# Performance work log

Hardware: AMD Instinct MI355X
Metric: run time of the kernel (lower is better)

## Reference

```python
import jax, jax.numpy as jnp
import numpy as np

B, S, IN_DIM, D, H, L = 2, 2048, 64, 512, 8, 2
DK = D // H
EPS = 1e-5

def _layernorm(x, g, b):
    mu = jnp.mean(x, axis=-1, keepdims=True)
    var = jnp.mean((x - mu) ** 2, axis=-1, keepdims=True)
    return (x - mu) * jax.lax.rsqrt(var + EPS) * g + b

def _prob_sparse_layer(x, Wq, bq, Wk, bk, Wv, bv, fcW, fcb, ln_g, ln_b):
    # x: [B, S, D]
    Bs, Ss, _ = x.shape
    Q = (x @ Wq + bq).reshape(Bs, Ss, H, DK).transpose(0, 2, 1, 3)  # [B,H,S,DK]
    K = (x @ Wk + bk).reshape(Bs, Ss, H, DK).transpose(0, 2, 1, 3)
    V = (x @ Wv + bv).reshape(Bs, Ss, H, DK).transpose(0, 2, 1, 3)
    scores = jnp.einsum('bhqd,bhkd->bhqk', Q, K) / np.sqrt(DK).astype(np.float32)
    k = max(1, Ss // 10)
    top_scores, _ = jax.lax.top_k(scores, k)          # [B,H,S,k]
    threshold = top_scores[..., -1:]                  # k-th largest per row
    sparse_scores = jnp.where(scores < threshold, -jnp.inf, scores)
    attn = jax.nn.softmax(sparse_scores, axis=-1)     # dropout is identity in eval
    out = jnp.einsum('bhqk,bhkd->bhqd', attn, V)
    out = out.transpose(0, 2, 1, 3).reshape(Bs, Ss, D)
    out = out @ fcW + fcb
    return _layernorm(x + out, ln_g, ln_b)

def setup_inputs() -> dict:
    key = jax.random.key(0)
    ks = jax.random.split(key, 16)
    sd = 1.0 / np.sqrt(D)
    sdi = 1.0 / np.sqrt(IN_DIM)
    return {
        'x': jax.random.normal(ks[0], (B, S, IN_DIM), jnp.float32),
        'enc_W': jax.random.normal(ks[1], (IN_DIM, D), jnp.float32) * sdi,
        'enc_b': jnp.zeros((D,), jnp.float32),
        'Wq': jax.random.normal(ks[2], (L, D, D), jnp.float32) * sd,
        'bq': jnp.zeros((L, D), jnp.float32),
        'Wk': jax.random.normal(ks[3], (L, D, D), jnp.float32) * sd,
        'bk': jnp.zeros((L, D), jnp.float32),
        'Wv': jax.random.normal(ks[4], (L, D, D), jnp.float32) * sd,
        'bv': jnp.zeros((L, D), jnp.float32),
        'fcW': jax.random.normal(ks[5], (L, D, D), jnp.float32) * sd,
        'fcb': jnp.zeros((L, D), jnp.float32),
        'ln_g': jnp.ones((L, D), jnp.float32),
        'ln_b': jnp.zeros((L, D), jnp.float32),
        'dec_W': jax.random.normal(ks[6], (D, IN_DIM), jnp.float32) * sd,
        'dec_b': jnp.zeros((IN_DIM,), jnp.float32),
    }

def reference(x, enc_W, enc_b, Wq, bq, Wk, bk, Wv, bv, fcW, fcb, ln_g, ln_b, dec_W, dec_b):
    h = x @ enc_W + enc_b  # [B,S,D]
    for i in range(Wq.shape[0]):
        h = _prob_sparse_layer(h, Wq[i], bq[i], Wk[i], bk[i], Wv[i], bv[i],
                               fcW[i], fcb[i], ln_g[i], ln_b[i])
    return h[:, -1, :] @ dec_W + dec_b  # [B, IN_DIM]
```

## Files before the change

### kernel.cpp

```cpp
#include <hip/hip_runtime.h>
#include <hip/hip_bf16.h>

typedef unsigned short u16;
typedef __bf16 bf16x8 __attribute__((ext_vector_type(8)));
typedef u16 u16x8 __attribute__((ext_vector_type(8)));
typedef float f32x4 __attribute__((ext_vector_type(4)));

#define S_LEN 2048
#define NH 8
#define DMODEL 512
#define TOPK 204

__device__ __forceinline__ u16 f2b(float f) {
  __hip_bfloat16 h = __float2bfloat16(f);
  return __builtin_bit_cast(u16, h);
}
__device__ __forceinline__ unsigned kmap16(u16 b) {
  return (unsigned)(u16)(b ^ ((b & 0x8000) ? 0xFFFFu : 0x8000u));
}
__device__ __forceinline__ float kunmap(unsigned k) {
  unsigned tb = (k & 0x8000u) ? (k ^ 0x8000u) : (~k & 0xFFFFu);
  return __uint_as_float(tb << 16);
}

__global__ void transpose_w(const float* __restrict__ in, u16* __restrict__ out, int R, int C) {
  __shared__ float tile[32][33];
  int c0 = blockIdx.x * 32, r0 = blockIdx.y * 32;
  int tx = threadIdx.x & 31, ty = threadIdx.x >> 5;
#pragma unroll
  for (int i = 0; i < 32; i += 8)
    tile[ty + i][tx] = in[(long long)(r0 + ty + i) * C + c0 + tx];
  __syncthreads();
#pragma unroll
  for (int i = 0; i < 32; i += 8)
    out[(long long)(c0 + ty + i) * R + r0 + tx] = f2b(tile[tx][ty + i]);
}

__global__ void transpose_w4(const float* __restrict__ W0, const float* __restrict__ W1,
                             const float* __restrict__ W2, const float* __restrict__ W3,
                             u16* __restrict__ O0, u16* __restrict__ O1,
                             u16* __restrict__ O2, u16* __restrict__ O3) {
  __shared__ float tile[32][33];
  const float* in;
  u16* out;
  switch (blockIdx.z) {
    case 0: in = W0; out = O0; break;
    case 1: in = W1; out = O1; break;
    case 2: in = W2; out = O2; break;
    default: in = W3; out = O3; break;
  }
  int c0 = blockIdx.x * 32, r0 = blockIdx.y * 32;
  int tx = threadIdx.x & 31, ty = threadIdx.x >> 5;
#pragma unroll
  for (int i = 0; i < 32; i += 8)
    tile[ty + i][tx] = in[(long long)(r0 + ty + i) * 512 + c0 + tx];
  __syncthreads();
#pragma unroll
  for (int i = 0; i < 32; i += 8)
    out[(long long)(c0 + ty + i) * 512 + r0 + tx] = f2b(tile[tx][ty + i]);
}

__global__ void conv_b(const float* __restrict__ in, u16* __restrict__ out, int n) {
  int i = blockIdx.x * 256 + threadIdx.x;
  if (i < n) out[i] = f2b(i < n ? in[i] : 0.f);
}

template <int MODE>
__global__ __launch_bounds__(256) void gemm_bt(
    const u16* __restrict__ A, const u16* __restrict__ BT, const float* __restrict__ bias,
    float* __restrict__ outF, u16* __restrict__ outB,
    int M, int N, int K, float scale) {
  __shared__ u16 As[64 * 32];
  __shared__ u16 Bs[128 * 32];
  int n0 = blockIdx.x * 128, m0 = blockIdx.y * 64;
  int t = threadIdx.x;
  int lane = t & 63, wv = t >> 6;
  int mw = (wv & 1) * 32, nw = (wv >> 1) * 64;
  int fr = lane & 15, fg = lane >> 4;
  f32x4 acc[2][4] = {};
  for (int kt = 0; kt < K; kt += 32) {
    int e0 = t * 8;
    int r0r = e0 >> 5, c0c = e0 & 31;
    int e1 = e0 + 2048;
    int r1r = e1 >> 5, c1c = e1 & 31;
    *(u16x8*)&As[e0] = *(const u16x8*)&A[(long long)(m0 + r0r) * K + kt + c0c];
    *(u16x8*)&Bs[e0] = *(const u16x8*)&BT[(long long)(n0 + r0r) * K + kt + c0c];
    *(u16x8*)&Bs[e1] = *(const u16x8*)&BT[(long long)(n0 + r1r) * K + kt + c1c];
    __syncthreads();
    bf16x8 af[2], bfv[4];
#pragma unroll
    for (int i = 0; i < 2; i++) af[i] = *(const bf16x8*)&As[(mw + i * 16 + fr) * 32 + fg * 8];
#pragma unroll
    for (int j = 0; j < 4; j++) bfv[j] = *(const bf16x8*)&Bs[(nw + j * 16 + fr) * 32 + fg * 8];
#pragma unroll
    for (int i = 0; i < 2; i++)
#pragma unroll
      for (int j = 0; j < 4; j++)
        acc[i][j] = __builtin_amdgcn_mfma_f32_16x16x32_bf16(af[i], bfv[j], acc[i][j], 0, 0, 0);
    __syncthreads();
  }
#pragma unroll
  for (int i = 0; i < 2; i++)
#pragma unroll
    for (int j = 0; j < 4; j++) {
      int mloc = mw + i * 16 + fg * 4;
      int n = n0 + nw + j * 16 + fr;
      float bvl = bias ? bias[n] : 0.f;
#pragma unroll
      for (int r = 0; r < 4; r++) {
        int m = m0 + mloc + r;
        float v = acc[i][j][r] * scale + bvl;
        if constexpr (MODE == 0) {
          outF[(long long)m * N + n] = v;
        } else if constexpr (MODE == 4) {
          outF[(long long)m * N + n] = v;
          outB[(long long)m * N + n] = f2b(v);
        } else if constexpr (MODE == 2) {
          outB[(long long)((m >> 11) * NH + (n >> 6)) * (S_LEN * 64) + (long long)(m & 2047) * 64 + (n & 63)] = f2b(v);
        } else if constexpr (MODE == 3) {
          outB[((long long)((m >> 11) * NH + (n >> 6)) * 64 + (n & 63)) * S_LEN + (m & 2047)] = f2b(v);
        }
      }
    }
}

__global__ __launch_bounds__(512) void score_pv(
    const u16* __restrict__ Qb, const u16* __restrict__ Kb, const u16* __restrict__ VTb,
    u16* __restrict__ aoB) {
  __shared__ u16 Qs[16 * 64];
  __shared__ u16 Ss[16 * 2048];
  __shared__ unsigned lokeyS[16];
  __shared__ float mS[16];
  __shared__ float zS[8 * 16];
  int bh = blockIdx.y, m0 = blockIdx.x * 16, t = threadIdx.x;
  int lane = t & 63, wv = t >> 6, fr = lane & 15, fg = lane >> 4;
  const u16* Qg = Qb + ((long long)bh * S_LEN + m0) * 64;
  const u16* Kg = Kb + (long long)bh * S_LEN * 64;
  const u16* Vg = VTb + (long long)bh * 64 * S_LEN;
  if (t < 128) {
    int row = t >> 3, cc = t & 7;
    *(u16x8*)&Qs[row * 64 + ((cc ^ (row & 7)) * 8)] = *(const u16x8*)&Qg[row * 64 + cc * 8];
  }
  __syncthreads();
  bf16x8 aq[2];
#pragma unroll
  for (int ks = 0; ks < 2; ks++)
    aq[ks] = *(const bf16x8*)&Qs[fr * 64 + (((fg + 4 * ks) ^ (fr & 7)) * 8)];

#pragma unroll 4
  for (int tt = 0; tt < 16; tt++) {
    int col0 = wv * 256 + tt * 16;
    f32x4 acc = {};
#pragma unroll
    for (int ks = 0; ks < 2; ks++) {
      bf16x8 bk = *(const bf16x8*)&Kg[(long long)(col0 + fr) * 64 + ks * 32 + fg * 8];
      acc = __builtin_amdgcn_mfma_f32_16x16x32_bf16(aq[ks], bk, acc, 0, 0, 0);
    }
#pragma unroll
    for (int r = 0; r < 4; r++) {
      float s = acc[r] * 0.125f;
      u16 key = (u16)kmap16(f2b(s));
      int row = fg * 4 + r;
      Ss[row * 2048 + ((col0 + fr) ^ ((row & 15) << 3))] = key;
    }
  }
  __syncthreads();

  for (int rr = wv * 2; rr < wv * 2 + 2; rr++) {
    const unsigned* cu = (const unsigned*)&Ss[rr * 2048];
    unsigned k32[32];
#pragma unroll
    for (int j = 0; j < 16; j++) {
      unsigned w = cu[lane + 64 * j];
      k32[2 * j] = w & 0xFFFFu;
      k32[2 * j + 1] = w >> 16;
    }
    unsigned mx = 0;
#pragma unroll
    for (int j = 0; j < 32; j++) mx = max(mx, k32[j]);
#pragma unroll
    for (int o = 1; o < 64; o <<= 1) mx = max(mx, (unsigned)__shfl_xor((int)mx, o));
    unsigned lo = 0, hi = mx;
    while (lo < hi) {
      unsigned mid = (lo + hi + 1) >> 1;
      int c = 0;
#pragma unroll
      for (int j = 0; j < 32; j++)
        c += (int)__popcll(__ballot(k32[j] >= mid));
      if (c >= TOPK) lo = mid; else hi = mid - 1;
    }
    if (lane == 0) {
      lokeyS[rr] = lo;
      mS[rr] = kunmap(mx);
    }
  }
  __syncthreads();

  unsigned myLo = lokeyS[fr];
  float myM = mS[fr];
  float zpart = 0.f;
  f32x4 acc_o[4] = {};
#pragma unroll 2
  for (int step = 0; step < 8; step++) {
    int k0 = wv * 256 + step * 32;
    u16x8 kk = *(const u16x8*)&Ss[fr * 2048 + ((k0 + fg * 8) ^ ((fr & 15) << 3))];
    u16x8 wpa;
#pragma unroll
    for (int e = 0; e < 8; e++) {
      unsigned key = kk[e];
      float pv = 0.f;
      if (key >= myLo) pv = __expf(kunmap(key) - myM);
      zpart += pv;
      wpa[e] = f2b(pv);
    }
    bf16x8 pa = *(bf16x8*)&wpa;
#pragma unroll
    for (int j = 0; j < 4; j++) {
      bf16x8 bv = *(const bf16x8*)&Vg[(long long)(j * 16 + fr) * 2048 + k0 + fg * 8];
      acc_o[j] = __builtin_amdgcn_mfma_f32_16x16x32_bf16(pa, bv, acc_o[j], 0, 0, 0);
    }
  }
  zpart += __shfl_xor(zpart, 16);
  zpart += __shfl_xor(zpart, 32);
  __syncthreads();

  float* Of = (float*)Ss;
#pragma unroll
  for (int j = 0; j < 4; j++)
#pragma unroll
    for (int r = 0; r < 4; r++)
      Of[wv * 1024 + (fg * 4 + r) * 64 + j * 16 + fr] = acc_o[j][r];
  if (fg == 0) zS[wv * 16 + fr] = zpart;
  __syncthreads();
  long long ob = (long long)(bh >> 3) * S_LEN * DMODEL + (bh & 7) * 64;
#pragma unroll
  for (int o = t; o < 1024; o += 512) {
    int row = o >> 6, dk = o & 63;
    float s = 0.f;
#pragma unroll
    for (int w = 0; w < 8; w++) s += Of[w * 1024 + o];
    float z = 0.f;
#pragma unroll
    for (int w = 0; w < 8; w++) z += zS[w * 16 + row];
    aoB[ob + (long long)(m0 + row) * DMODEL + dk] = f2b(s / z);
  }
}

__global__ __launch_bounds__(256) void resid_ln(const float* __restrict__ h, const float* __restrict__ fco,
                                                const float* __restrict__ g, const float* __restrict__ b,
                                                float* __restrict__ hout, u16* __restrict__ hbout) {
  __shared__ float red[4];
  int row = blockIdx.x;
  int t = threadIdx.x;
  long long base = (long long)row * 512;
  float v0 = h[base + t] + fco[base + t];
  float v1 = h[base + t + 256] + fco[base + t + 256];
  float s = v0 + v1;
#pragma unroll
  for (int o = 32; o > 0; o >>= 1) s += __shfl_down(s, o);
  if ((t & 63) == 0) red[t >> 6] = s;
  __syncthreads();
  float mu = (red[0] + red[1] + red[2] + red[3]) * (1.f / 512.f);
  float d0 = v0 - mu, d1 = v1 - mu;
  float q = d0 * d0 + d1 * d1;
#pragma unroll
  for (int o = 32; o > 0; o >>= 1) q += __shfl_down(q, o);
  __syncthreads();
  if ((t & 63) == 0) red[t >> 6] = q;
  __syncthreads();
  float var = (red[0] + red[1] + red[2] + red[3]) * (1.f / 512.f);
  float rs = rsqrtf(var + 1e-5f);
  float y0 = d0 * rs * g[t] + b[t];
  float y1 = d1 * rs * g[t + 256] + b[t + 256];
  hout[base + t] = y0;
  hout[base + t + 256] = y1;
  hbout[base + t] = f2b(y0);
  hbout[base + t + 256] = f2b(y1);
}

__global__ void decoder_k(const float* __restrict__ h, const float* __restrict__ W,
                          const float* __restrict__ bias, float* __restrict__ out) {
  int t = threadIdx.x;
  int b = t >> 6, j = t & 63;
  const float* hr = h + ((long long)b * S_LEN + (S_LEN - 1)) * DMODEL;
  float s = 0.f;
  for (int d = 0; d < DMODEL; d++) s += hr[d] * W[(long long)d * 64 + j];
  out[t] = s + bias[j];
}

extern "C" void kernel_launch(void* const* d_in, const int* in_sizes, int n_in,
                              void* d_out, int out_size, void* d_ws, size_t ws_size,
                              hipStream_t stream) {
  const float* x = (const float*)d_in[0];
  const float* enc_W = (const float*)d_in[1];
  const float* enc_b = (const float*)d_in[2];
  const float* Wq = (const float*)d_in[3];
  const float* bq = (const float*)d_in[4];
  const float* Wk = (const float*)d_in[5];
  const float* bk = (const float*)d_in[6];
  const float* Wv = (const float*)d_in[7];
  const float* bv = (const float*)d_in[8];
  const float* fcW = (const float*)d_in[9];
  const float* fcb = (const float*)d_in[10];
  const float* ln_g = (const float*)d_in[11];
  const float* ln_b = (const float*)d_in[12];
  const float* dec_W = (const float*)d_in[13];
  const float* dec_b = (const float*)d_in[14];

  char* p = (char*)d_ws;
  auto alloc = [&](size_t bytes) {
    char* r = p;
    p += (bytes + 255) & ~(size_t)255;
    return r;
  };
  const size_t BS = 2 * (size_t)S_LEN;
  u16* encWT = (u16*)alloc(512 * 64 * 2);
  u16* xbf = (u16*)alloc(BS * 64 * 2);
  float* hF = (float*)alloc(BS * 512 * 4);
  u16* hB = (u16*)alloc(BS * 512 * 2);
  u16* WqT = (u16*)alloc(512 * 512 * 2);
  u16* WkT = (u16*)alloc(512 * 512 * 2);
  u16* WvT = (u16*)alloc(512 * 512 * 2);
  u16* fcWT = (u16*)alloc(512 * 512 * 2);
  u16* Qb = (u16*)alloc((size_t)16 * 2048 * 64 * 2);
  u16* Kb = (u16*)alloc((size_t)16 * 2048 * 64 * 2);
  u16* VTb = (u16*)alloc((size_t)16 * 2048 * 64 * 2);
  u16* aoB = (u16*)alloc(BS * 512 * 2);
  float* fcO = (float*)Qb;

  transpose_w<<<dim3(16, 2), 256, 0, stream>>>(enc_W, encWT, 64, 512);
  conv_b<<<(int)(BS * 64 / 256), 256, 0, stream>>>(x, xbf, (int)(BS * 64));
  gemm_bt<4><<<dim3(4, 64), 256, 0, stream>>>(xbf, encWT, enc_b, hF, hB, 4096, 512, 64, 1.f);

  for (int l = 0; l < 2; l++) {
    transpose_w4<<<dim3(16, 16, 4), 256, 0, stream>>>(
        Wq + (size_t)l * 512 * 512, Wk + (size_t)l * 512 * 512,
        Wv + (size_t)l * 512 * 512, fcW + (size_t)l * 512 * 512,
        WqT, WkT, WvT, fcWT);
    gemm_bt<2><<<dim3(4, 64), 256, 0, stream>>>(hB, WqT, bq + l * 512, nullptr, Qb, 4096, 512, 512, 1.f);
    gemm_bt<2><<<dim3(4, 64), 256, 0, stream>>>(hB, WkT, bk + l * 512, nullptr, Kb, 4096, 512, 512, 1.f);
    gemm_bt<3><<<dim3(4, 64), 256, 0, stream>>>(hB, WvT, bv + l * 512, nullptr, VTb, 4096, 512, 512, 1.f);
    score_pv<<<dim3(128, 16), 512, 0, stream>>>(Qb, Kb, VTb, aoB);
    gemm_bt<0><<<dim3(4, 64), 256, 0, stream>>>(aoB, fcWT, fcb + l * 512, fcO, nullptr, 4096, 512, 512, 1.f);
    resid_ln<<<4096, 256, 0, stream>>>(hF, fcO, ln_g + l * 512, ln_b + l * 512, hF, hB);
  }
  decoder_k<<<1, 128, 0, stream>>>(hF, dec_W, dec_b, (float*)d_out);
}
```

Before: 447.5 us.

## Fuse QKV projections into one GEMM and double score_pv waves per block

Replaces three separate Q, K and V projection launches with one GEMM over N=1536. It picks the bias and the output layout per 512-column segment. This relies on WqT, WkT and WvT being laid out contiguously in memory. The attention kernel now runs 1024 threads per block, so each wave handles one row's top-k binary search and half as many score and PV columns. The partial-output reduction goes through a swizzled shared buffer to avoid bank conflicts. The aim is fewer launches, better reuse of the A tile, and more parallelism in the selection phase, at the cost of higher register pressure and a wider cross-wave reduction.

```diff
diff --git a/kernel.cpp b/kernel.cpp
--- a/kernel.cpp
+++ b/kernel.cpp
@@ -62,13 +62,14 @@
 
 __global__ void conv_b(const float* __restrict__ in, u16* __restrict__ out, int n) {
   int i = blockIdx.x * 256 + threadIdx.x;
-  if (i < n) out[i] = f2b(i < n ? in[i] : 0.f);
+  if (i < n) out[i] = f2b(in[i]);
 }
 
 template <int MODE>
 __global__ __launch_bounds__(256) void gemm_bt(
-    const u16* __restrict__ A, const u16* __restrict__ BT, const float* __restrict__ bias,
-    float* __restrict__ outF, u16* __restrict__ outB,
+    const u16* __restrict__ A, const u16* __restrict__ BT,
+    const float* __restrict__ bias, const float* __restrict__ biasK, const float* __restrict__ biasV,
+    float* __restrict__ outF, u16* __restrict__ outB, u16* __restrict__ outBK, u16* __restrict__ outBV,
     int M, int N, int K, float scale) {
   __shared__ u16 As[64 * 32];
   __shared__ u16 Bs[128 * 32];
@@ -105,7 +106,13 @@
     for (int j = 0; j < 4; j++) {
       int mloc = mw + i * 16 + fg * 4;
       int n = n0 + nw + j * 16 + fr;
-      float bvl = bias ? bias[n] : 0.f;
+      float bvl;
+      if constexpr (MODE == 5) {
+        int seg = n >> 9, nn = n & 511;
+        bvl = (seg == 0 ? bias : seg == 1 ? biasK : biasV)[nn];
+      } else {
+        bvl = bias ? bias[n] : 0.f;
+      }
 #pragma unroll
       for (int r = 0; r < 4; r++) {
         int m = m0 + mloc + r;
@@ -115,23 +122,30 @@
         } else if constexpr (MODE == 4) {
           outF[(long long)m * N + n] = v;
           outB[(long long)m * N + n] = f2b(v);
-        } else if constexpr (MODE == 2) {
-          outB[(long long)((m >> 11) * NH + (n >> 6)) * (S_LEN * 64) + (long long)(m & 2047) * 64 + (n & 63)] = f2b(v);
-        } else if constexpr (MODE == 3) {
-          outB[((long long)((m >> 11) * NH + (n >> 6)) * 64 + (n & 63)) * S_LEN + (m & 2047)] = f2b(v);
+        } else if constexpr (MODE == 5) {
+          int seg = n >> 9, nn = n & 511;
+          u16 val = f2b(v);
+          if (seg == 2) {
+            outBV[((long long)((m >> 11) * NH + (nn >> 6)) * 64 + (nn & 63)) * S_LEN + (m & 2047)] = val;
+          } else {
+            long long qkidx = (long long)((m >> 11) * NH + (nn >> 6)) * (S_LEN * 64) +
+                              (long long)(m & 2047) * 64 + (nn & 63);
+            if (seg == 0) outB[qkidx] = val;
+            else outBK[qkidx] = val;
+          }
         }
       }
     }
 }
 
-__global__ __launch_bounds__(512) void score_pv(
+__global__ __launch_bounds__(1024, 8) void score_pv(
     const u16* __restrict__ Qb, const u16* __restrict__ Kb, const u16* __restrict__ VTb,
     u16* __restrict__ aoB) {
   __shared__ u16 Qs[16 * 64];
-  __shared__ u16 Ss[16 * 2048];
+  __shared__ __align__(16) u16 Ss[16 * 2048];
   __shared__ unsigned lokeyS[16];
   __shared__ float mS[16];
-  __shared__ float zS[8 * 16];
+  __shared__ float zS[16 * 16];
   int bh = blockIdx.y, m0 = blockIdx.x * 16, t = threadIdx.x;
   int lane = t & 63, wv = t >> 6, fr = lane & 15, fg = lane >> 4;
   const u16* Qg = Qb + ((long long)bh * S_LEN + m0) * 64;
@@ -148,8 +162,8 @@
     aq[ks] = *(const bf16x8*)&Qs[fr * 64 + (((fg + 4 * ks) ^ (fr & 7)) * 8)];
 
 #pragma unroll 4
-  for (int tt = 0; tt < 16; tt++) {
-    int col0 = wv * 256 + tt * 16;
+  for (int tt = 0; tt < 8; tt++) {
+    int col0 = wv * 128 + tt * 16;
     f32x4 acc = {};
 #pragma unroll
     for (int ks = 0; ks < 2; ks++) {
@@ -166,7 +180,8 @@
   }
   __syncthreads();
 
-  for (int rr = wv * 2; rr < wv * 2 + 2; rr++) {
+  {
+    int rr = wv;
     const unsigned* cu = (const unsigned*)&Ss[rr * 2048];
     unsigned k32[32];
 #pragma unroll
@@ -201,8 +216,8 @@
   float zpart = 0.f;
   f32x4 acc_o[4] = {};
 #pragma unroll 2
-  for (int step = 0; step < 8; step++) {
-    int k0 = wv * 256 + step * 32;
+  for (int step = 0; step < 4; step++) {
+    int k0 = wv * 128 + step * 32;
     u16x8 kk = *(const u16x8*)&Ss[fr * 2048 + ((k0 + fg * 8) ^ ((fr & 15) << 3))];
     u16x8 wpa;
 #pragma unroll
@@ -228,20 +243,22 @@
 #pragma unroll
   for (int j = 0; j < 4; j++)
 #pragma unroll
-    for (int r = 0; r < 4; r++)
-      Of[wv * 1024 + (fg * 4 + r) * 64 + j * 16 + fr] = acc_o[j][r];
+    for (int r = 0; r < 4; r++) {
+      int row = fg * 4 + r, col = j * 16 + fr;
+      Of[wv * 1024 + row * 64 + (col ^ ((row >> 2) << 3))] = acc_o[j][r];
+    }
   if (fg == 0) zS[wv * 16 + fr] = zpart;
   __syncthreads();
   long long ob = (long long)(bh >> 3) * S_LEN * DMODEL + (bh & 7) * 64;
-#pragma unroll
-  for (int o = t; o < 1024; o += 512) {
-    int row = o >> 6, dk = o & 63;
+  {
+    int row = t >> 6, dk = t & 63;
+    int sw = dk ^ ((row >> 2) << 3);
     float s = 0.f;
 #pragma unroll
-    for (int w = 0; w < 8; w++) s += Of[w * 1024 + o];
+    for (int w = 0; w < 16; w++) s += Of[w * 1024 + row * 64 + sw];
     float z = 0.f;
 #pragma unroll
-    for (int w = 0; w < 8; w++) z += zS[w * 16 + row];
+    for (int w = 0; w < 16; w++) z += zS[w * 16 + row];
     aoB[ob + (long long)(m0 + row) * DMODEL + dk] = f2b(s / z);
   }
 }
@@ -330,18 +347,19 @@
 
   transpose_w<<<dim3(16, 2), 256, 0, stream>>>(enc_W, encWT, 64, 512);
   conv_b<<<(int)(BS * 64 / 256), 256, 0, stream>>>(x, xbf, (int)(BS * 64));
-  gemm_bt<4><<<dim3(4, 64), 256, 0, stream>>>(xbf, encWT, enc_b, hF, hB, 4096, 512, 64, 1.f);
+  gemm_bt<4><<<dim3(4, 64), 256, 0, stream>>>(xbf, encWT, enc_b, nullptr, nullptr,
+                                              hF, hB, nullptr, nullptr, 4096, 512, 64, 1.f);
 
   for (int l = 0; l < 2; l++) {
     transpose_w4<<<dim3(16, 16, 4), 256, 0, stream>>>(
         Wq + (size_t)l * 512 * 512, Wk + (size_t)l * 512 * 512,
         Wv + (size_t)l * 512 * 512, fcW + (size_t)l * 512 * 512,
         WqT, WkT, WvT, fcWT);
-    gemm_bt<2><<<dim3(4, 64), 256, 0, stream>>>(hB, WqT, bq + l * 512, nullptr, Qb, 4096, 512, 512, 1.f);
-    gemm_bt<2><<<dim3(4, 64), 256, 0, stream>>>(hB, WkT, bk + l * 512, nullptr, Kb, 4096, 512, 512, 1.f);
-    gemm_bt<3><<<dim3(4, 64), 256, 0, stream>>>(hB, WvT, bv + l * 512, nullptr, VTb, 4096, 512, 512, 1.f);
-    score_pv<<<dim3(128, 16), 512, 0, stream>>>(Qb, Kb, VTb, aoB);
-    gemm_bt<0><<<dim3(4, 64), 256, 0, stream>>>(aoB, fcWT, fcb + l * 512, fcO, nullptr, 4096, 512, 512, 1.f);
+    gemm_bt<5><<<dim3(12, 64), 256, 0, stream>>>(hB, WqT, bq + l * 512, bk + l * 512, bv + l * 512,
+                                                 nullptr, Qb, Kb, VTb, 4096, 1536, 512, 1.f);
+    score_pv<<<dim3(128, 16), 1024, 0, stream>>>(Qb, Kb, VTb, aoB);
+    gemm_bt<0><<<dim3(4, 64), 256, 0, stream>>>(aoB, fcWT, fcb + l * 512, nullptr, nullptr,
+                                                fcO, nullptr, nullptr, nullptr, 4096, 512, 512, 1.f);
     resid_ln<<<4096, 256, 0, stream>>>(hF, fcO, ln_g + l * 512, ln_b + l * 512, hF, hB);
   }
   decoder_k<<<1, 128, 0, stream>>>(hF, dec_W, dec_b, (float*)d_out);
```

Result: faster. 411.5 us (-8.0%).
